# Performance work log

Measured on AMD Instinct MI355X. Metric: run time of the kernel, lower is better.

## Reference

```python
import jax, jax.numpy as jnp
import numpy as np

N_VIEWS = 8


def _trilinear(vol, pts):
    """Trilinear interpolation of vol [Nx,Ny,Nz] at pts [...,3] (voxel coords), zero outside."""
    nx, ny, nz = vol.shape
    x, y, z = pts[..., 0], pts[..., 1], pts[..., 2]
    x0f, y0f, z0f = jnp.floor(x), jnp.floor(y), jnp.floor(z)
    fx, fy, fz = x - x0f, y - y0f, z - z0f
    x0 = x0f.astype(jnp.int32)
    y0 = y0f.astype(jnp.int32)
    z0 = z0f.astype(jnp.int32)
    out = jnp.zeros(x.shape, vol.dtype)
    for dx in (0, 1):
        wx = fx if dx else (1.0 - fx)
        ix = x0 + dx
        vx = (ix >= 0) & (ix < nx)
        ixc = jnp.clip(ix, 0, nx - 1)
        for dy in (0, 1):
            wy = fy if dy else (1.0 - fy)
            iy = y0 + dy
            vxy = vx & (iy >= 0) & (iy < ny)
            iyc = jnp.clip(iy, 0, ny - 1)
            for dz in (0, 1):
                wz = fz if dz else (1.0 - fz)
                iz = z0 + dz
                valid = vxy & (iz >= 0) & (iz < nz)
                izc = jnp.clip(iz, 0, nz - 1)
                v = vol[ixc, iyc, izc]  # irregular gather
                out = out + jnp.where(valid, v, jnp.zeros((), vol.dtype)) * (wx * wy * wz)
    return out


def cone_project(vol, src_pos, det_center, det_u_vec, det_v_vec,
                 det_u, det_v, du, dv, voxel_spacing, n_steps):
    """Cone-beam forward projection: ray-march src->detector pixel, trilinear sampling."""
    nx, ny, nz = vol.shape
    us = (jnp.arange(det_u, dtype=vol.dtype) - (det_u - 1) / 2.0) * du
    vs = (jnp.arange(det_v, dtype=vol.dtype) - (det_v - 1) / 2.0) * dv
    # detector pixel world positions: [V, U, W, 3]
    det_pts = (det_center[:, None, None, :]
               + us[None, :, None, None] * det_u_vec[:, None, None, :]
               + vs[None, None, :, None] * det_v_vec[:, None, None, :])
    src = src_pos[:, None, None, :]            # [V,1,1,3]
    diff = det_pts - src                        # [V,U,W,3]
    ray_len = jnp.sqrt(jnp.sum(diff * diff, axis=-1))  # [V,U,W]
    step_len = ray_len / n_steps
    center = (jnp.array([nx, ny, nz], dtype=vol.dtype) - 1.0) / 2.0
    fracs = (jnp.arange(n_steps, dtype=vol.dtype) + 0.5) / n_steps

    def body(acc, s):
        p = src + s * diff                      # world coords [V,U,W,3]
        vox = p / voxel_spacing + center        # voxel coords
        return acc + _trilinear(vol, vox), None

    acc, _ = jax.lax.scan(body, jnp.zeros(ray_len.shape, vol.dtype), fracs)
    return acc * step_len


def setup_inputs() -> dict:
    key = jax.random.key(0)
    k1, k2 = jax.random.split(key)
    vol_shape = (256, 256, 256)
    x = 0.1 * jax.random.normal(k1, vol_shape, dtype=jnp.float32)
    reco = 0.1 * jax.random.normal(k2, vol_shape, dtype=jnp.float32)
    # circular cone-beam trajectory (units = voxels, spacing 1.0)
    sad, sdd = 400.0, 800.0  # source-axis / source-detector distance
    angles = np.linspace(0.0, np.pi, N_VIEWS, endpoint=False)
    ca, sa = np.cos(angles), np.sin(angles)
    zeros = np.zeros(N_VIEWS)
    src_pos = np.stack([-sad * ca, -sad * sa, zeros], axis=-1)
    det_center = np.stack([(sdd - sad) * ca, (sdd - sad) * sa, zeros], axis=-1)
    det_u_vec = np.stack([-sa, ca, zeros], axis=-1)
    det_v_vec = np.tile(np.array([0.0, 0.0, 1.0]), (N_VIEWS, 1))
    return {
        "x": x,
        "reco": reco,
        "src_pos": jnp.asarray(src_pos, jnp.float32),
        "det_center": jnp.asarray(det_center, jnp.float32),
        "det_u_vec": jnp.asarray(det_u_vec, jnp.float32),
        "det_v_vec": jnp.asarray(det_v_vec, jnp.float32),
        "du": 3.0,
        "dv": 3.0,
        "voxel_spacing": 1.0,
        "det_u": 128,
        "det_v": 128,
        "n_steps": 192,
    }


def reference(x, reco, src_pos, det_center, det_u_vec, det_v_vec,
              du, dv, voxel_spacing, det_u, det_v, n_steps):
    updated = x + reco
    sino = cone_project(updated, src_pos, det_center, det_u_vec, det_v_vec,
                        det_u, det_v, du, dv, voxel_spacing, n_steps)
    return sino, jax.nn.relu(updated)
```

## Files before the change

kernel.cpp:

```cpp
#include <hip/hip_runtime.h>
#include <math.h>

typedef float nfloat4 __attribute__((ext_vector_type(4)));

__global__ __launch_bounds__(256) void add_relu_kernel(
    const float* __restrict__ x,
    const float* __restrict__ reco,
    float* __restrict__ relu_out,
    float* __restrict__ upd_out,
    int n4)
{
    int i = blockIdx.x * blockDim.x + threadIdx.x;
    int stride = gridDim.x * blockDim.x;
    const nfloat4* x4 = (const nfloat4*)x;
    const nfloat4* r4 = (const nfloat4*)reco;
    nfloat4* ro4 = (nfloat4*)relu_out;
    nfloat4* uo4 = (nfloat4*)upd_out;
    for (; i < n4; i += stride) {
        nfloat4 a = x4[i];
        nfloat4 b = r4[i];
        nfloat4 u = a + b;
        if (uo4) uo4[i] = u;
        nfloat4 r;
        r.x = fmaxf(u.x, 0.f); r.y = fmaxf(u.y, 0.f);
        r.z = fmaxf(u.z, 0.f); r.w = fmaxf(u.w, 0.f);
        ro4[i] = r;
    }
}

template <int TWO>
__device__ __forceinline__ float fetch_corner(
    const float* __restrict__ vol_a,
    const float* __restrict__ vol_b,
    int ix, int iy, int iz,
    int nx, int ny, int nz)
{
    bool valid = (ix >= 0) & (ix < nx) & (iy >= 0) & (iy < ny) &
                 (iz >= 0) & (iz < nz);
    if (!valid) return 0.0f;
    int idx = (ix * ny + iy) * nz + iz;
    float v = vol_a[idx];
    if (TWO) v += vol_b[idx];
    return v;
}

__device__ __forceinline__ void clip_axis(float a, float b, float lo, float hi,
                                          float& t_lo, float& t_hi)
{
    if (fabsf(b) > 1e-6f) {
        float t0 = (lo - a) / b;
        float t1 = (hi - a) / b;
        float tmn = fminf(t0, t1);
        float tmx = fmaxf(t0, t1);
        t_lo = fmaxf(t_lo, tmn);
        t_hi = fminf(t_hi, tmx);
    } else {
        if (a <= lo || a >= hi) { t_lo = 1.0f; t_hi = 0.0f; }
    }
}

template <int TWO>
__global__ __launch_bounds__(256) void cone_project_seg_kernel(
    const float* __restrict__ vol_a,
    const float* __restrict__ vol_b,
    const float* __restrict__ src_pos,
    const float* __restrict__ det_center,
    const float* __restrict__ det_u_vec,
    const float* __restrict__ det_v_vec,
    const float* __restrict__ du_p,
    const float* __restrict__ dv_p,
    const float* __restrict__ spacing_p,
    const int* __restrict__ det_u_p,
    const int* __restrict__ det_v_p,
    const int* __restrict__ nsteps_p,
    float* __restrict__ sino,
    int n_views, int nx, int ny, int nz)
{
    const int det_u = *det_u_p;
    const int det_v = *det_v_p;
    const int n_steps = *nsteps_p;
    const float du = *du_p;
    const float dv = *dv_p;
    const float inv_sp = 1.0f / *spacing_p;

    const long total = (long)n_views * det_u * det_v;
    const int pix = threadIdx.x & 63;
    const int seg = threadIdx.x >> 6;
    const long idx = (long)blockIdx.x * 64 + pix;
    const bool live = idx < total;

    const long cidx = live ? idx : 0;
    const int v = (int)(cidx % det_v);
    const int u = (int)((cidx / det_v) % det_u);
    const int view = (int)(cidx / ((long)det_u * det_v));

    const float us = ((float)u - (det_u - 1) * 0.5f) * du;
    const float vs = ((float)v - (det_v - 1) * 0.5f) * dv;

    const float sx = src_pos[view * 3 + 0];
    const float sy = src_pos[view * 3 + 1];
    const float sz = src_pos[view * 3 + 2];

    const float dpx = det_center[view * 3 + 0] + us * det_u_vec[view * 3 + 0] + vs * det_v_vec[view * 3 + 0];
    const float dpy = det_center[view * 3 + 1] + us * det_u_vec[view * 3 + 1] + vs * det_v_vec[view * 3 + 1];
    const float dpz = det_center[view * 3 + 2] + us * det_u_vec[view * 3 + 2] + vs * det_v_vec[view * 3 + 2];

    const float dx = dpx - sx;
    const float dy = dpy - sy;
    const float dz = dpz - sz;
    const float ray_len = sqrtf(dx * dx + dy * dy + dz * dz);
    const float step_len = ray_len / (float)n_steps;

    const float cx = (nx - 1) * 0.5f;
    const float cy = (ny - 1) * 0.5f;
    const float cz = (nz - 1) * 0.5f;

    float t_lo = 0.0f, t_hi = 1.0f;
    clip_axis(sx * inv_sp + cx, dx * inv_sp, -1.0f, (float)nx, t_lo, t_hi);
    clip_axis(sy * inv_sp + cy, dy * inv_sp, -1.0f, (float)ny, t_lo, t_hi);
    clip_axis(sz * inv_sp + cz, dz * inv_sp, -1.0f, (float)nz, t_lo, t_hi);

    int i_min = 0, i_max = -1;
    if (t_hi > t_lo) {
        i_min = (int)floorf(t_lo * (float)n_steps - 0.5f) - 1;
        i_max = (int)ceilf(t_hi * (float)n_steps - 0.5f) + 1;
        i_min = max(i_min, 0);
        i_max = min(i_max, n_steps - 1);
    }
    if (!live) { i_min = 0; i_max = -1; }

    const int count = i_max - i_min + 1;
    const int per = (count + 3) >> 2;
    const int is = i_min + seg * per;
    const int ie = min(is + per - 1, i_max);

    const float inv_n = 1.0f / (float)n_steps;
    const int snz = ny * nz;

    float acc = 0.0f;
    for (int i = is; i <= ie; ++i) {
        const float s = ((float)i + 0.5f) * inv_n;
        const float px = fmaf(s, dx, sx) * inv_sp + cx;
        const float py = fmaf(s, dy, sy) * inv_sp + cy;
        const float pz = fmaf(s, dz, sz) * inv_sp + cz;

        const float x0f = floorf(px);
        const float y0f = floorf(py);
        const float z0f = floorf(pz);
        const float fx = px - x0f;
        const float fy = py - y0f;
        const float fz = pz - z0f;
        const int x0 = (int)x0f;
        const int y0 = (int)y0f;
        const int z0 = (int)z0f;

        const float gx = 1.0f - fx;
        const float gy = 1.0f - fy;
        const float gz = 1.0f - fz;

        const bool interior = (x0 >= 0) & (x0 + 1 < nx) &
                              (y0 >= 0) & (y0 + 1 < ny) &
                              (z0 >= 0) & (z0 + 1 < nz);

        float samp = 0.0f;
        if (interior) {
            const int base = (x0 * ny + y0) * nz + z0;
            const float* pa = vol_a + base;
            float v000 = pa[0];
            float v001 = pa[1];
            float v010 = pa[nz];
            float v011 = pa[nz + 1];
            float v100 = pa[snz];
            float v101 = pa[snz + 1];
            float v110 = pa[snz + nz];
            float v111 = pa[snz + nz + 1];
            if (TWO) {
                const float* pb = vol_b + base;
                v000 += pb[0];
                v001 += pb[1];
                v010 += pb[nz];
                v011 += pb[nz + 1];
                v100 += pb[snz];
                v101 += pb[snz + 1];
                v110 += pb[snz + nz];
                v111 += pb[snz + nz + 1];
            }
            samp = fmaf(gx * gy * gz, v000, samp);
            samp = fmaf(gx * gy * fz, v001, samp);
            samp = fmaf(gx * fy * gz, v010, samp);
            samp = fmaf(gx * fy * fz, v011, samp);
            samp = fmaf(fx * gy * gz, v100, samp);
            samp = fmaf(fx * gy * fz, v101, samp);
            samp = fmaf(fx * fy * gz, v110, samp);
            samp = fmaf(fx * fy * fz, v111, samp);
        } else {
            samp = fmaf(gx * gy * gz, fetch_corner<TWO>(vol_a, vol_b, x0,     y0,     z0,     nx, ny, nz), samp);
            samp = fmaf(gx * gy * fz, fetch_corner<TWO>(vol_a, vol_b, x0,     y0,     z0 + 1, nx, ny, nz), samp);
            samp = fmaf(gx * fy * gz, fetch_corner<TWO>(vol_a, vol_b, x0,     y0 + 1, z0,     nx, ny, nz), samp);
            samp = fmaf(gx * fy * fz, fetch_corner<TWO>(vol_a, vol_b, x0,     y0 + 1, z0 + 1, nx, ny, nz), samp);
            samp = fmaf(fx * gy * gz, fetch_corner<TWO>(vol_a, vol_b, x0 + 1, y0,     z0,     nx, ny, nz), samp);
            samp = fmaf(fx * gy * fz, fetch_corner<TWO>(vol_a, vol_b, x0 + 1, y0,     z0 + 1, nx, ny, nz), samp);
            samp = fmaf(fx * fy * gz, fetch_corner<TWO>(vol_a, vol_b, x0 + 1, y0 + 1, z0,     nx, ny, nz), samp);
            samp = fmaf(fx * fy * fz, fetch_corner<TWO>(vol_a, vol_b, x0 + 1, y0 + 1, z0 + 1, nx, ny, nz), samp);
        }
        acc += samp;
    }

    __shared__ float red[256];
    red[threadIdx.x] = acc;
    __syncthreads();
    if (seg == 0 && live) {
        float tot = red[pix] + red[pix + 64] + red[pix + 128] + red[pix + 192];
        sino[idx] = tot * step_len;
    }
}

extern "C" void kernel_launch(void* const* d_in, const int* in_sizes, int n_in,
                              void* d_out, int out_size, void* d_ws, size_t ws_size,
                              hipStream_t stream) {
    const float* x          = (const float*)d_in[0];
    const float* reco       = (const float*)d_in[1];
    const float* src_pos    = (const float*)d_in[2];
    const float* det_center = (const float*)d_in[3];
    const float* det_u_vec  = (const float*)d_in[4];
    const float* det_v_vec  = (const float*)d_in[5];
    const float* du_p       = (const float*)d_in[6];
    const float* dv_p       = (const float*)d_in[7];
    const float* spacing_p  = (const float*)d_in[8];
    const int*   det_u_p    = (const int*)d_in[9];
    const int*   det_v_p    = (const int*)d_in[10];
    const int*   nsteps_p   = (const int*)d_in[11];

    const int n_vol = in_sizes[0];
    const int n_views = in_sizes[2] / 3;

    int n = 1;
    while ((long)(n + 1) * (n + 1) * (n + 1) <= (long)n_vol) ++n;
    const int nx = n, ny = n, nz = n;

    const int sino_size = out_size - n_vol;
    float* sino     = (float*)d_out;
    float* relu_out = (float*)d_out + sino_size;

    const bool use_ws = ws_size >= (size_t)n_vol * sizeof(float);
    float* upd = (float*)d_ws;

    const int n4 = n_vol / 4;
    add_relu_kernel<<<2048, 256, 0, stream>>>(
        x, reco, relu_out, use_ws ? upd : nullptr, n4);

    const int blocks = (sino_size + 63) / 64;
    if (use_ws) {
        cone_project_seg_kernel<0><<<blocks, 256, 0, stream>>>(
            upd, nullptr,
            src_pos, det_center, det_u_vec, det_v_vec,
            du_p, dv_p, spacing_p, det_u_p, det_v_p, nsteps_p,
            sino, n_views, nx, ny, nz);
    } else {
        cone_project_seg_kernel<1><<<blocks, 256, 0, stream>>>(
            x, reco,
            src_pos, det_center, det_u_vec, det_v_vec,
            du_p, dv_p, spacing_p, det_u_p, det_v_p, nsteps_p,
            sino, n_views, nx, ny, nz);
    }
}
```

Baseline: 234.8 us.

## Interleave two branchless ray segments per thread and swizzle blocks across views

Each thread now marches two interleaved ray segments (8 segments per pixel instead of 4), and trilinear sampling is branchless: indices are clamped and out-of-range corners get zero weight. This is meant to expose more independent gathers per thread and remove divergence between interior and boundary samples. Block IDs are swizzled so consecutive blocks span different views, and launch bounds request 4 blocks per CU. In exchange, every step issues all 8 (or 16) loads even for invalid steps, and register pressure rises.

```diff
diff --git a/kernel.cpp b/kernel.cpp
--- a/kernel.cpp
+++ b/kernel.cpp
@@ -28,22 +28,6 @@
     }
 }
 
-template <int TWO>
-__device__ __forceinline__ float fetch_corner(
-    const float* __restrict__ vol_a,
-    const float* __restrict__ vol_b,
-    int ix, int iy, int iz,
-    int nx, int ny, int nz)
-{
-    bool valid = (ix >= 0) & (ix < nx) & (iy >= 0) & (iy < ny) &
-                 (iz >= 0) & (iz < nz);
-    if (!valid) return 0.0f;
-    int idx = (ix * ny + iy) * nz + iz;
-    float v = vol_a[idx];
-    if (TWO) v += vol_b[idx];
-    return v;
-}
-
 __device__ __forceinline__ void clip_axis(float a, float b, float lo, float hi,
                                           float& t_lo, float& t_hi)
 {
@@ -60,7 +44,98 @@
 }
 
 template <int TWO>
-__global__ __launch_bounds__(256) void cone_project_seg_kernel(
+__device__ __forceinline__ float sample_step(
+    const float* __restrict__ vol_a,
+    const float* __restrict__ vol_b,
+    float s,
+    float sx, float sy, float sz,
+    float dx, float dy, float dz,
+    float inv_sp, float cx, float cy, float cz,
+    int nx, int ny, int nz, bool live_step)
+{
+    const float px = fmaf(s, dx, sx) * inv_sp + cx;
+    const float py = fmaf(s, dy, sy) * inv_sp + cy;
+    const float pz = fmaf(s, dz, sz) * inv_sp + cz;
+
+    const float x0f = floorf(px);
+    const float y0f = floorf(py);
+    const float z0f = floorf(pz);
+    const float fx = px - x0f;
+    const float fy = py - y0f;
+    const float fz = pz - z0f;
+    const int x0 = (int)x0f;
+    const int y0 = (int)y0f;
+    const int z0 = (int)z0f;
+
+    const bool vx0 = (unsigned)x0 < (unsigned)nx;
+    const bool vx1 = (unsigned)(x0 + 1) < (unsigned)nx;
+    const bool vy0 = (unsigned)y0 < (unsigned)ny;
+    const bool vy1 = (unsigned)(y0 + 1) < (unsigned)ny;
+    const bool vz0 = live_step & ((unsigned)z0 < (unsigned)nz);
+    const bool vz1 = live_step & ((unsigned)(z0 + 1) < (unsigned)nz);
+
+    const int xc0 = min(max(x0, 0), nx - 1);
+    const int xc1 = min(max(x0 + 1, 0), nx - 1);
+    const int yc0 = min(max(y0, 0), ny - 1);
+    const int yc1 = min(max(y0 + 1, 0), ny - 1);
+    const int zc0 = min(max(z0, 0), nz - 1);
+    const int zc1 = min(max(z0 + 1, 0), nz - 1);
+
+    const int r00 = (xc0 * ny + yc0) * nz;
+    const int r01 = (xc0 * ny + yc1) * nz;
+    const int r10 = (xc1 * ny + yc0) * nz;
+    const int r11 = (xc1 * ny + yc1) * nz;
+
+    float v000 = vol_a[r00 + zc0];
+    float v001 = vol_a[r00 + zc1];
+    float v010 = vol_a[r01 + zc0];
+    float v011 = vol_a[r01 + zc1];
+    float v100 = vol_a[r10 + zc0];
+    float v101 = vol_a[r10 + zc1];
+    float v110 = vol_a[r11 + zc0];
+    float v111 = vol_a[r11 + zc1];
+    if (TWO) {
+        v000 += vol_b[r00 + zc0];
+        v001 += vol_b[r00 + zc1];
+        v010 += vol_b[r01 + zc0];
+        v011 += vol_b[r01 + zc1];
+        v100 += vol_b[r10 + zc0];
+        v101 += vol_b[r10 + zc1];
+        v110 += vol_b[r11 + zc0];
+        v111 += vol_b[r11 + zc1];
+    }
+
+    const float gx = 1.0f - fx;
+    const float gy = 1.0f - fy;
+    const float gz = 1.0f - fz;
+    const float wxy00 = gx * gy;
+    const float wxy01 = gx * fy;
+    const float wxy10 = fx * gy;
+    const float wxy11 = fx * fy;
+
+    const float w000 = (vx0 & vy0 & vz0) ? wxy00 * gz : 0.0f;
+    const float w001 = (vx0 & vy0 & vz1) ? wxy00 * fz : 0.0f;
+    const float w010 = (vx0 & vy1 & vz0) ? wxy01 * gz : 0.0f;
+    const float w011 = (vx0 & vy1 & vz1) ? wxy01 * fz : 0.0f;
+    const float w100 = (vx1 & vy0 & vz0) ? wxy10 * gz : 0.0f;
+    const float w101 = (vx1 & vy0 & vz1) ? wxy10 * fz : 0.0f;
+    const float w110 = (vx1 & vy1 & vz0) ? wxy11 * gz : 0.0f;
+    const float w111 = (vx1 & vy1 & vz1) ? wxy11 * fz : 0.0f;
+
+    float samp = 0.0f;
+    samp = fmaf(w000, v000, samp);
+    samp = fmaf(w001, v001, samp);
+    samp = fmaf(w010, v010, samp);
+    samp = fmaf(w011, v011, samp);
+    samp = fmaf(w100, v100, samp);
+    samp = fmaf(w101, v101, samp);
+    samp = fmaf(w110, v110, samp);
+    samp = fmaf(w111, v111, samp);
+    return samp;
+}
+
+template <int TWO>
+__global__ __launch_bounds__(256, 4) void cone_project_seg_kernel(
     const float* __restrict__ vol_a,
     const float* __restrict__ vol_b,
     const float* __restrict__ src_pos,
@@ -86,7 +161,14 @@
     const long total = (long)n_views * det_u * det_v;
     const int pix = threadIdx.x & 63;
     const int seg = threadIdx.x >> 6;
-    const long idx = (long)blockIdx.x * 64 + pix;
+
+    int bid = blockIdx.x;
+    if ((gridDim.x & 7) == 0) {
+        const int cpx = (int)(gridDim.x >> 3);
+        bid = (bid & 7) * cpx + (bid >> 3);
+    }
+
+    const long idx = (long)bid * 64 + pix;
     const bool live = idx < total;
 
     const long cidx = live ? idx : 0;
@@ -130,81 +212,27 @@
     if (!live) { i_min = 0; i_max = -1; }
 
     const int count = i_max - i_min + 1;
-    const int per = (count + 3) >> 2;
-    const int is = i_min + seg * per;
-    const int ie = min(is + per - 1, i_max);
+    const int per8 = (count + 7) >> 3;
+    const int isA = i_min + seg * per8;
+    const int isB = i_min + (seg + 4) * per8;
+    const int ieA = min(isA + per8 - 1, i_max);
+    const int ieB = min(isB + per8 - 1, i_max);
 
     const float inv_n = 1.0f / (float)n_steps;
-    const int snz = ny * nz;
-
-    float acc = 0.0f;
-    for (int i = is; i <= ie; ++i) {
-        const float s = ((float)i + 0.5f) * inv_n;
-        const float px = fmaf(s, dx, sx) * inv_sp + cx;
-        const float py = fmaf(s, dy, sy) * inv_sp + cy;
-        const float pz = fmaf(s, dz, sz) * inv_sp + cz;
-
-        const float x0f = floorf(px);
-        const float y0f = floorf(py);
-        const float z0f = floorf(pz);
-        const float fx = px - x0f;
-        const float fy = py - y0f;
-        const float fz = pz - z0f;
-        const int x0 = (int)x0f;
-        const int y0 = (int)y0f;
-        const int z0 = (int)z0f;
-
-        const float gx = 1.0f - fx;
-        const float gy = 1.0f - fy;
-        const float gz = 1.0f - fz;
-
-        const bool interior = (x0 >= 0) & (x0 + 1 < nx) &
-                              (y0 >= 0) & (y0 + 1 < ny) &
-                              (z0 >= 0) & (z0 + 1 < nz);
-
-        float samp = 0.0f;
-        if (interior) {
-            const int base = (x0 * ny + y0) * nz + z0;
-            const float* pa = vol_a + base;
-            float v000 = pa[0];
-            float v001 = pa[1];
-            float v010 = pa[nz];
-            float v011 = pa[nz + 1];
-            float v100 = pa[snz];
-            float v101 = pa[snz + 1];
-            float v110 = pa[snz + nz];
-            float v111 = pa[snz + nz + 1];
-            if (TWO) {
-                const float* pb = vol_b + base;
-                v000 += pb[0];
-                v001 += pb[1];
-                v010 += pb[nz];
-                v011 += pb[nz + 1];
-                v100 += pb[snz];
-                v101 += pb[snz + 1];
-                v110 += pb[snz + nz];
-                v111 += pb[snz + nz + 1];
-            }
-            samp = fmaf(gx * gy * gz, v000, samp);
-            samp = fmaf(gx * gy * fz, v001, samp);
-            samp = fmaf(gx * fy * gz, v010, samp);
-            samp = fmaf(gx * fy * fz, v011, samp);
-            samp = fmaf(fx * gy * gz, v100, samp);
-            samp = fmaf(fx * gy * fz, v101, samp);
-            samp = fmaf(fx * fy * gz, v110, samp);
-            samp = fmaf(fx * fy * fz, v111, samp);
-        } else {
-            samp = fmaf(gx * gy * gz, fetch_corner<TWO>(vol_a, vol_b, x0,     y0,     z0,     nx, ny, nz), samp);
-            samp = fmaf(gx * gy * fz, fetch_corner<TWO>(vol_a, vol_b, x0,     y0,     z0 + 1, nx, ny, nz), samp);
-            samp = fmaf(gx * fy * gz, fetch_corner<TWO>(vol_a, vol_b, x0,     y0 + 1, z0,     nx, ny, nz), samp);
-            samp = fmaf(gx * fy * fz, fetch_corner<TWO>(vol_a, vol_b, x0,     y0 + 1, z0 + 1, nx, ny, nz), samp);
-            samp = fmaf(fx * gy * gz, fetch_corner<TWO>(vol_a, vol_b, x0 + 1, y0,     z0,     nx, ny, nz), samp);
-            samp = fmaf(fx * gy * fz, fetch_corner<TWO>(vol_a, vol_b, x0 + 1, y0,     z0 + 1, nx, ny, nz), samp);
-            samp = fmaf(fx * fy * gz, fetch_corner<TWO>(vol_a, vol_b, x0 + 1, y0 + 1, z0,     nx, ny, nz), samp);
-            samp = fmaf(fx * fy * fz, fetch_corner<TWO>(vol_a, vol_b, x0 + 1, y0 + 1, z0 + 1, nx, ny, nz), samp);
-        }
-        acc += samp;
-    }
+
+    float accA = 0.0f;
+    float accB = 0.0f;
+    for (int j = 0; j < per8; ++j) {
+        const int iA = isA + j;
+        const int iB = isB + j;
+        const float sA = ((float)iA + 0.5f) * inv_n;
+        const float sB = ((float)iB + 0.5f) * inv_n;
+        accA += sample_step<TWO>(vol_a, vol_b, sA, sx, sy, sz, dx, dy, dz,
+                                 inv_sp, cx, cy, cz, nx, ny, nz, iA <= ieA);
+        accB += sample_step<TWO>(vol_a, vol_b, sB, sx, sy, sz, dx, dy, dz,
+                                 inv_sp, cx, cy, cz, nx, ny, nz, iB <= ieB);
+    }
+    const float acc = accA + accB;
 
     __shared__ float red[256];
     red[threadIdx.x] = acc;
```

Measured after the change: 237.4 us. About the same (+1.1%).
